# Kernel optimization log

Measured on AMD Instinct MI355X. Metric: run time of the kernel, lower is better.

The kernel has to match this reference:

```python
import jax, jax.numpy as jnp
import numpy as np

SEG_NUM = 100000
D_SEG = 128
D_S = 258       # 2*D_SEG + 2 (offset)
D_M7 = 512
D_M8 = 256
MASK = 64
T_SLOTS = 96
B = 4096
CAND_OUT = 4            # candidate_layer out_features
DW_COLS = D_M8 - CAND_OUT  # 252
BN_EPS = 1e-6
COS_EPS = 1e-8


def setup_inputs() -> dict:
    key = jax.random.key(0)
    ks = jax.random.split(key, 20)
    s = 0.02
    return {
        "src": jax.random.randint(ks[0], (B,), 0, SEG_NUM),
        "dest": jax.random.randint(ks[1], (B,), 0, SEG_NUM),
        "t": jax.random.randint(ks[2], (B,), 0, T_SLOTS),
        "candidates": jax.random.randint(ks[3], (B, MASK), 0, SEG_NUM),
        "offset": jax.random.normal(ks[4], (B, 4), jnp.float32),
        "emb_feat": jax.random.normal(ks[5], (SEG_NUM, D_SEG), jnp.float32) * s,
        "emb_dest": jax.random.normal(ks[6], (SEG_NUM, D_SEG), jnp.float32) * s,
        "w1": jax.random.normal(ks[7], (D_M7, D_S), jnp.float32) * s,
        "b1": jnp.zeros((D_M7,), jnp.float32),
        "bn_gamma": jnp.ones((D_M7,), jnp.float32),
        "bn_beta": jnp.zeros((D_M7,), jnp.float32),
        "bn_mean": jax.random.normal(ks[8], (D_M7,), jnp.float32) * s,
        "bn_var": jax.random.uniform(ks[9], (D_M7,), jnp.float32, 0.5, 1.5),
        "w2": jax.random.normal(ks[10], (D_M8, D_M7), jnp.float32) * s,
        "b2": jnp.zeros((D_M8,), jnp.float32),
        "dense_w": jax.random.normal(ks[11], (SEG_NUM, DW_COLS), jnp.float32) * s,
        "dense_b": jnp.zeros((SEG_NUM,), jnp.float32),
        "cand_w": jax.random.normal(ks[12], (CAND_OUT, 2), jnp.float32) * s,
        "cand_b": jnp.zeros((CAND_OUT,), jnp.float32),
        "segs_src": jax.random.normal(ks[13], (SEG_NUM, 2), jnp.float32),
        "segs_trg": jax.random.normal(ks[14], (SEG_NUM, 2), jnp.float32),
        "traffic_pop": jax.random.uniform(ks[15], (SEG_NUM, T_SLOTS), jnp.float32),
    }


def reference(src, dest, t, candidates, offset, emb_feat, emb_dest, w1, b1,
              bn_gamma, bn_beta, bn_mean, bn_var, w2, b2, dense_w, dense_b,
              cand_w, cand_b, segs_src, segs_trg, traffic_pop):
    # --- ODEncoder: embedding gathers + offset features ---
    code = jnp.concatenate([emb_feat[src], emb_dest[dest], offset[:, 1:3]], axis=1)  # [B, 258]
    # --- MLP: Linear -> BatchNorm1d (eval, running stats) -> ReLU -> Linear ---
    h = code @ w1.T + b1
    h = (h - bn_mean) * (bn_gamma / jnp.sqrt(bn_var + BN_EPS)) + bn_beta
    h = jax.nn.relu(h)
    out = h @ w2.T + b2  # [B, 256]
    # --- gather dense rows by candidate index ---
    sub_w = dense_w[candidates]   # [B, M, 252]
    sub_b = dense_b[candidates]   # [B, M]
    # --- traffic feature: traffic_pop[candidate, t] ---
    traffic_feat = traffic_pop[candidates, t[:, None]]  # [B, M]
    # --- cosine similarity between dest-direction and segment direction ---
    v1 = segs_src[dest][:, None, :] - segs_src[candidates]  # [B, M, 2]
    v2 = segs_trg[candidates] - segs_src[candidates]        # [B, M, 2]
    num = jnp.sum(v1 * v2, axis=-1)
    den = jnp.maximum(jnp.linalg.norm(v1, axis=-1) * jnp.linalg.norm(v2, axis=-1), COS_EPS)
    cos_feat = num / den  # [B, M]
    cand_feat = jnp.stack([cos_feat, traffic_feat], axis=-1)  # [B, M, 2]
    emb_cand = cand_feat @ cand_w.T + cand_b                  # [B, M, 4]
    W = jnp.concatenate([sub_w, emb_cand], axis=-1)           # [B, M, 256]
    # --- batched small matvec + bias ---
    logits = jnp.einsum('bmd,bd->bm', W, out) + sub_b         # [B, M]
    return logits
```

## Files before the change

### kernel.cpp

```cpp
#include <hip/hip_runtime.h>


#define BATCH 4096
#define DSEG 128
#define DS_ 258
#define DM7 512
#define DM8 256
#define NCAND 64
#define DWC 252
#define TSLOTS 96

typedef short bf16x8 __attribute__((ext_vector_type(8)));
typedef float f32x4 __attribute__((ext_vector_type(4)));

static __device__ __forceinline__ short f2bf(float f) {
    union { float f; unsigned u; } v; v.f = f;
    unsigned r = (v.u + 0x7FFFu + ((v.u >> 16) & 1u)) >> 16;
    return (short)r;
}

__global__ __launch_bounds__(512) void mlp_mfma_kernel(
    const int* __restrict__ src, const int* __restrict__ dest,
    const float* __restrict__ offset,
    const float* __restrict__ emb_feat, const float* __restrict__ emb_dest,
    const float* __restrict__ w1, const float* __restrict__ b1,
    const float* __restrict__ bn_gamma, const float* __restrict__ bn_beta,
    const float* __restrict__ bn_mean, const float* __restrict__ bn_var,
    const float* __restrict__ w2, const float* __restrict__ b2,
    float* __restrict__ out_ws)
{
    __shared__ __align__(16) short hlds[16][520];
    const int tid = threadIdx.x;
    const int w    = tid >> 6;
    const int lane = tid & 63;
    const int lg   = lane >> 4;
    const int lr   = lane & 15;
    const int b0   = blockIdx.x * 16;

    const int si = src[b0 + lr];
    const int di = dest[b0 + lr];
    const float* fb = emb_feat + (size_t)si * DSEG;
    const float* db = emb_dest + (size_t)di * DSEG;
    bf16x8 a1[8];
#pragma unroll
    for (int s = 0; s < 8; ++s) {
        const float* p = (s < 4) ? (fb + s * 32 + lg * 8)
                                 : (db + (s - 4) * 32 + lg * 8);
        const float4 x = *(const float4*)p;
        const float4 y = *(const float4*)(p + 4);
        bf16x8 t;
        t[0] = f2bf(x.x); t[1] = f2bf(x.y); t[2] = f2bf(x.z); t[3] = f2bf(x.w);
        t[4] = f2bf(y.x); t[5] = f2bf(y.y); t[6] = f2bf(y.z); t[7] = f2bf(y.w);
        a1[s] = t;
    }
    float off1[4], off2[4];
#pragma unroll
    for (int q = 0; q < 4; ++q) {
        const float4 o = *(const float4*)(offset + (size_t)(b0 + lg * 4 + q) * 4);
        off1[q] = o.y; off2[q] = o.z;
    }

#pragma unroll
    for (int nt = 0; nt < 4; ++nt) {
        const int n = (w * 4 + nt) * 16 + lr;
        const float* wrow = w1 + (size_t)n * DS_;
        f32x4 acc = {0.f, 0.f, 0.f, 0.f};
#pragma unroll
        for (int s = 0; s < 8; ++s) {
            const float* p = wrow + s * 32 + lg * 8;
            const float2 x0 = *(const float2*)(p);
            const float2 x1 = *(const float2*)(p + 2);
            const float2 x2 = *(const float2*)(p + 4);
            const float2 x3 = *(const float2*)(p + 6);
            bf16x8 bb;
            bb[0] = f2bf(x0.x); bb[1] = f2bf(x0.y); bb[2] = f2bf(x1.x); bb[3] = f2bf(x1.y);
            bb[4] = f2bf(x2.x); bb[5] = f2bf(x2.y); bb[6] = f2bf(x3.x); bb[7] = f2bf(x3.y);
            acc = __builtin_amdgcn_mfma_f32_16x16x32_bf16(a1[s], bb, acc, 0, 0, 0);
        }
        const float2 wtail = *(const float2*)(wrow + 256);
        const float scale = bn_gamma[n] / sqrtf(bn_var[n] + 1e-6f);
        const float shift = bn_beta[n] - bn_mean[n] * scale;
        const float bias  = b1[n];
#pragma unroll
        for (int q = 0; q < 4; ++q) {
            float v = acc[q] + bias + off1[q] * wtail.x + off2[q] * wtail.y;
            v = fmaf(v, scale, shift);
            v = fmaxf(v, 0.f);
            hlds[lg * 4 + q][n] = f2bf(v);
        }
    }
    __syncthreads();

    bf16x8 a2[16];
#pragma unroll
    for (int s = 0; s < 16; ++s) {
        a2[s] = *(const bf16x8*)&hlds[lr][s * 32 + lg * 8];
    }
#pragma unroll
    for (int nt = 0; nt < 2; ++nt) {
        const int n = (w * 2 + nt) * 16 + lr;
        const float* wrow = w2 + (size_t)n * DM7;
        f32x4 acc = {0.f, 0.f, 0.f, 0.f};
#pragma unroll
        for (int s = 0; s < 16; ++s) {
            const float4 x = *(const float4*)(wrow + s * 32 + lg * 8);
            const float4 y = *(const float4*)(wrow + s * 32 + lg * 8 + 4);
            bf16x8 bb;
            bb[0] = f2bf(x.x); bb[1] = f2bf(x.y); bb[2] = f2bf(x.z); bb[3] = f2bf(x.w);
            bb[4] = f2bf(y.x); bb[5] = f2bf(y.y); bb[6] = f2bf(y.z); bb[7] = f2bf(y.w);
            acc = __builtin_amdgcn_mfma_f32_16x16x32_bf16(a2[s], bb, acc, 0, 0, 0);
        }
        const float bias = b2[n];
#pragma unroll
        for (int q = 0; q < 4; ++q) {
            out_ws[(size_t)(b0 + lg * 4 + q) * DM8 + n] = acc[q] + bias;
        }
    }
}

__global__ __launch_bounds__(256) void logits_kernel(
    const int* __restrict__ dest, const int* __restrict__ tt,
    const int* __restrict__ candidates,
    const float* __restrict__ dense_w, const float* __restrict__ dense_b,
    const float* __restrict__ cand_w, const float* __restrict__ cand_b,
    const float* __restrict__ segs_src, const float* __restrict__ segs_trg,
    const float* __restrict__ traffic_pop,
    const float* __restrict__ out_ws,
    float* __restrict__ logits)
{
    __shared__ float plds[4][16][67];
    const int b = blockIdx.x;
    const int tid = threadIdx.x;
    const int wave = tid >> 6;
    const int lane = tid & 63;
    const int mbase = wave * 16;

    int candv = 0;
    if (lane < 16) candv = candidates[b * NCAND + mbase + lane];

    const int ll = (lane < 63) ? lane : 62;
    float4 dw[16];
#pragma unroll
    for (int i = 0; i < 16; ++i) {
        const int ci = __shfl(candv, i, 64);
        dw[i] = *(const float4*)(dense_w + (size_t)ci * DWC + ll * 4);
    }

    float4 o4 = *(const float4*)(out_ws + (size_t)b * DM8 + ll * 4);
    if (lane == 63) { o4.x = 0.f; o4.y = 0.f; o4.z = 0.f; o4.w = 0.f; }

    float tail = 0.f;
    if (lane < 16) {
        const float4 t4 = *(const float4*)(out_ws + (size_t)b * DM8 + DWC);
        const int db = dest[b];
        const float2 dsx = *(const float2*)(segs_src + 2 * (size_t)db);
        const float2 sx = *(const float2*)(segs_src + 2 * (size_t)candv);
        const float2 tx = *(const float2*)(segs_trg + 2 * (size_t)candv);
        const float v1x = dsx.x - sx.x, v1y = dsx.y - sx.y;
        const float v2x = tx.x - sx.x, v2y = tx.y - sx.y;
        const float num = v1x * v2x + v1y * v2y;
        const float den = fmaxf(sqrtf(v1x * v1x + v1y * v1y) *
                                sqrtf(v2x * v2x + v2y * v2y), 1e-8f);
        const float cosv = num / den;
        const float tf = traffic_pop[(size_t)candv * TSLOTS + tt[b]];
        const float e0 = fmaf(cosv, cand_w[0], fmaf(tf, cand_w[1], cand_b[0]));
        const float e1 = fmaf(cosv, cand_w[2], fmaf(tf, cand_w[3], cand_b[1]));
        const float e2 = fmaf(cosv, cand_w[4], fmaf(tf, cand_w[5], cand_b[2]));
        const float e3 = fmaf(cosv, cand_w[6], fmaf(tf, cand_w[7], cand_b[3]));
        tail = e0 * t4.x + e1 * t4.y + e2 * t4.z + e3 * t4.w + dense_b[candv];
    }

#pragma unroll
    for (int i = 0; i < 16; ++i) {
        const float p = dw[i].x * o4.x + dw[i].y * o4.y + dw[i].z * o4.z + dw[i].w * o4.w;
        plds[wave][i][lane] = p;
    }
    __syncthreads();

    const int cc = lane >> 2;
    const int qq = lane & 3;
    float s = 0.f;
#pragma unroll
    for (int j = 0; j < 16; ++j) s += plds[wave][cc][qq * 16 + j];
    s += __shfl_xor(s, 1, 64);
    s += __shfl_xor(s, 2, 64);
    const float tl = __shfl(tail, cc, 64);
    if (qq == 0) logits[(size_t)b * NCAND + mbase + cc] = s + tl;
}

extern "C" void kernel_launch(void* const* d_in, const int* in_sizes, int n_in,
                              void* d_out, int out_size, void* d_ws, size_t ws_size,
                              hipStream_t stream) {
    const int*   src         = (const int*)d_in[0];
    const int*   dest        = (const int*)d_in[1];
    const int*   tt          = (const int*)d_in[2];
    const int*   candidates  = (const int*)d_in[3];
    const float* offset      = (const float*)d_in[4];
    const float* emb_feat    = (const float*)d_in[5];
    const float* emb_dest    = (const float*)d_in[6];
    const float* w1          = (const float*)d_in[7];
    const float* b1          = (const float*)d_in[8];
    const float* bn_gamma    = (const float*)d_in[9];
    const float* bn_beta     = (const float*)d_in[10];
    const float* bn_mean     = (const float*)d_in[11];
    const float* bn_var      = (const float*)d_in[12];
    const float* w2          = (const float*)d_in[13];
    const float* b2          = (const float*)d_in[14];
    const float* dense_w     = (const float*)d_in[15];
    const float* dense_b     = (const float*)d_in[16];
    const float* cand_w      = (const float*)d_in[17];
    const float* cand_b      = (const float*)d_in[18];
    const float* segs_src    = (const float*)d_in[19];
    const float* segs_trg    = (const float*)d_in[20];
    const float* traffic_pop = (const float*)d_in[21];

    float* out_ws = (float*)d_ws;
    float* logits = (float*)d_out;

    mlp_mfma_kernel<<<BATCH / 16, 512, 0, stream>>>(
        src, dest, offset, emb_feat, emb_dest,
        w1, b1, bn_gamma, bn_beta, bn_mean, bn_var, w2, b2, out_ws);

    logits_kernel<<<BATCH, 256, 0, stream>>>(
        dest, tt, candidates, dense_w, dense_b, cand_w, cand_b,
        segs_src, segs_trg, traffic_pop, out_ws, logits);
}
```

Baseline: 89.28 us.

## Convert dense_w table to bf16 in extra MLP blocks and gather bf16 rows

Extra blocks appended to the MLP kernel convert the whole dense_w table from fp32 to bf16 into workspace on every call. The logits kernel then gathers 8-byte bf16 rows instead of 16-byte fp32 rows, halving gather traffic. The cost is a full-table read and a half-size write each call, plus bf16 rounding error in the logits. It only runs when the workspace is large enough for the table.

```diff
diff --git a/kernel.cpp b/kernel.cpp
--- a/kernel.cpp
+++ b/kernel.cpp
@@ -9,8 +9,10 @@
 #define NCAND 64
 #define DWC 252
 #define TSLOTS 96
+#define SEGN 100000
 
 typedef short bf16x8 __attribute__((ext_vector_type(8)));
+typedef short bf16x4 __attribute__((ext_vector_type(4)));
 typedef float f32x4 __attribute__((ext_vector_type(4)));
 
 static __device__ __forceinline__ short f2bf(float f) {
@@ -18,8 +20,11 @@
     unsigned r = (v.u + 0x7FFFu + ((v.u >> 16) & 1u)) >> 16;
     return (short)r;
 }
-
-__global__ __launch_bounds__(512) void mlp_mfma_kernel(
+static __device__ __forceinline__ float bfu2f(unsigned u16hi) {
+    union { unsigned u; float f; } v; v.u = u16hi << 16; return v.f;
+}
+
+__global__ __launch_bounds__(512) void mlp_conv_kernel(
     const int* __restrict__ src, const int* __restrict__ dest,
     const float* __restrict__ offset,
     const float* __restrict__ emb_feat, const float* __restrict__ emb_dest,
@@ -27,10 +32,27 @@
     const float* __restrict__ bn_gamma, const float* __restrict__ bn_beta,
     const float* __restrict__ bn_mean, const float* __restrict__ bn_var,
     const float* __restrict__ w2, const float* __restrict__ b2,
+    const float* __restrict__ dense_w, short* __restrict__ wtab,
     float* __restrict__ out_ws)
 {
+    const int tid = threadIdx.x;
+
+    if (blockIdx.x >= BATCH / 16) {
+        const size_t nthr = (size_t)(gridDim.x - BATCH / 16) * 512;
+        const size_t g0 = (size_t)(blockIdx.x - BATCH / 16) * 512 + tid;
+        const float4* __restrict__ src4 = (const float4*)dense_w;
+        bf16x4* __restrict__ dst4 = (bf16x4*)wtab;
+        const size_t n4 = (size_t)SEGN * DWC / 4;
+        for (size_t i = g0; i < n4; i += nthr) {
+            const float4 v = src4[i];
+            bf16x4 s;
+            s[0] = f2bf(v.x); s[1] = f2bf(v.y); s[2] = f2bf(v.z); s[3] = f2bf(v.w);
+            dst4[i] = s;
+        }
+        return;
+    }
+
     __shared__ __align__(16) short hlds[16][520];
-    const int tid = threadIdx.x;
     const int w    = tid >> 6;
     const int lane = tid & 63;
     const int lg   = lane >> 4;
@@ -118,10 +140,12 @@
     }
 }
 
-__global__ __launch_bounds__(256) void logits_kernel(
+template <bool BF16TAB>
+__global__ __launch_bounds__(256) void logits_kernel_t(
     const int* __restrict__ dest, const int* __restrict__ tt,
     const int* __restrict__ candidates,
-    const float* __restrict__ dense_w, const float* __restrict__ dense_b,
+    const float* __restrict__ dense_w, const unsigned short* __restrict__ wtab,
+    const float* __restrict__ dense_b,
     const float* __restrict__ cand_w, const float* __restrict__ cand_b,
     const float* __restrict__ segs_src, const float* __restrict__ segs_trg,
     const float* __restrict__ traffic_pop,
@@ -139,11 +163,20 @@
     if (lane < 16) candv = candidates[b * NCAND + mbase + lane];
 
     const int ll = (lane < 63) ? lane : 62;
-    float4 dw[16];
-#pragma unroll
-    for (int i = 0; i < 16; ++i) {
-        const int ci = __shfl(candv, i, 64);
-        dw[i] = *(const float4*)(dense_w + (size_t)ci * DWC + ll * 4);
+    float4 dwf[16];
+    uint2  dwb[16];
+    if (BF16TAB) {
+#pragma unroll
+        for (int i = 0; i < 16; ++i) {
+            const int ci = __shfl(candv, i, 64);
+            dwb[i] = *(const uint2*)(wtab + (size_t)ci * DWC + ll * 4);
+        }
+    } else {
+#pragma unroll
+        for (int i = 0; i < 16; ++i) {
+            const int ci = __shfl(candv, i, 64);
+            dwf[i] = *(const float4*)(dense_w + (size_t)ci * DWC + ll * 4);
+        }
     }
 
     float4 o4 = *(const float4*)(out_ws + (size_t)b * DM8 + ll * 4);
@@ -172,7 +205,15 @@
 
 #pragma unroll
     for (int i = 0; i < 16; ++i) {
-        const float p = dw[i].x * o4.x + dw[i].y * o4.y + dw[i].z * o4.z + dw[i].w * o4.w;
+        float p;
+        if (BF16TAB) {
+            p =        bfu2f(dwb[i].x & 0xFFFFu)  * o4.x;
+            p = fmaf(  bfu2f(dwb[i].x >> 16),       o4.y, p);
+            p = fmaf(  bfu2f(dwb[i].y & 0xFFFFu),   o4.z, p);
+            p = fmaf(  bfu2f(dwb[i].y >> 16),       o4.w, p);
+        } else {
+            p = dwf[i].x * o4.x + dwf[i].y * o4.y + dwf[i].z * o4.z + dwf[i].w * o4.w;
+        }
         plds[wave][i][lane] = p;
     }
     __syncthreads();
@@ -215,13 +256,25 @@
     const float* traffic_pop = (const float*)d_in[21];
 
     float* out_ws = (float*)d_ws;
+    const size_t OUT_WS_BYTES = (size_t)BATCH * DM8 * 4;
+    const size_t WTAB_BYTES = (size_t)SEGN * DWC * 2;
+    short* wtab = (short*)((char*)d_ws + OUT_WS_BYTES);
+    const bool use_bf16 = ws_size >= OUT_WS_BYTES + WTAB_BYTES;
     float* logits = (float*)d_out;
 
-    mlp_mfma_kernel<<<BATCH / 16, 512, 0, stream>>>(
+    const int nblk = use_bf16 ? (BATCH / 16) * 2 : (BATCH / 16);
+    mlp_conv_kernel<<<nblk, 512, 0, stream>>>(
         src, dest, offset, emb_feat, emb_dest,
-        w1, b1, bn_gamma, bn_beta, bn_mean, bn_var, w2, b2, out_ws);
-
-    logits_kernel<<<BATCH, 256, 0, stream>>>(
-        dest, tt, candidates, dense_w, dense_b, cand_w, cand_b,
-        segs_src, segs_trg, traffic_pop, out_ws, logits);
-}
+        w1, b1, bn_gamma, bn_beta, bn_mean, bn_var, w2, b2,
+        dense_w, wtab, out_ws);
+
+    if (use_bf16) {
+        logits_kernel_t<true><<<BATCH, 256, 0, stream>>>(
+            dest, tt, candidates, dense_w, (const unsigned short*)wtab, dense_b,
+            cand_w, cand_b, segs_src, segs_trg, traffic_pop, out_ws, logits);
+    } else {
+        logits_kernel_t<false><<<BATCH, 256, 0, stream>>>(
+            dest, tt, candidates, dense_w, (const unsigned short*)wtab, dense_b,
+            cand_w, cand_b, segs_src, segs_trg, traffic_pop, out_ws, logits);
+    }
+}
```

Result: faster. 86.39 us (-3.2%).

## Partition dense_w rows across blocks and bucket candidate hits to stream gathers

Applied to the files above, without the earlier changes.

Replaces the per-batch-row logits kernel with 256 blocks that each own a contiguous range of dense_w rows. Every block scans the whole candidates array, collects the hits that fall in its range into an LDS list, and computes logits with a wave-wide reduction per hit. The aim is better locality for the dense_w gathers, since each block touches only its own slice. In exchange every block rereads the full 1 MB candidates array, the LDS atomics serialize, and any hits beyond LISTCAP are silently dropped, so correctness depends on the input distribution.

```diff
diff --git a/kernel.cpp b/kernel.cpp
--- a/kernel.cpp
+++ b/kernel.cpp
@@ -9,6 +9,11 @@
 #define NCAND 64
 #define DWC 252
 #define TSLOTS 96
+#define SEGN 100000
+#define SBLK 256
+#define STHR 1024
+#define ROWS_PER_BLK 391
+#define LISTCAP 2560
 
 typedef short bf16x8 __attribute__((ext_vector_type(8)));
 typedef float f32x4 __attribute__((ext_vector_type(4)));
@@ -19,7 +24,7 @@
     return (short)r;
 }
 
-__global__ __launch_bounds__(512) void mlp_mfma_kernel(
+__global__ __launch_bounds__(512) void mlp_kernel(
     const int* __restrict__ src, const int* __restrict__ dest,
     const float* __restrict__ offset,
     const float* __restrict__ emb_feat, const float* __restrict__ emb_dest,
@@ -118,7 +123,7 @@
     }
 }
 
-__global__ __launch_bounds__(256) void logits_kernel(
+__global__ __launch_bounds__(1024) void logits_stream_kernel(
     const int* __restrict__ dest, const int* __restrict__ tt,
     const int* __restrict__ candidates,
     const float* __restrict__ dense_w, const float* __restrict__ dense_b,
@@ -128,64 +133,99 @@
     const float* __restrict__ out_ws,
     float* __restrict__ logits)
 {
-    __shared__ float plds[4][16][67];
-    const int b = blockIdx.x;
+    __shared__ int nhits;
+    __shared__ unsigned list_i[LISTCAP];
+    __shared__ int      list_s[LISTCAP];
+    __shared__ float    list_t[LISTCAP];
     const int tid = threadIdx.x;
-    const int wave = tid >> 6;
-    const int lane = tid & 63;
-    const int mbase = wave * 16;
-
-    int candv = 0;
-    if (lane < 16) candv = candidates[b * NCAND + mbase + lane];
-
-    const int ll = (lane < 63) ? lane : 62;
-    float4 dw[16];
-#pragma unroll
-    for (int i = 0; i < 16; ++i) {
-        const int ci = __shfl(candv, i, 64);
-        dw[i] = *(const float4*)(dense_w + (size_t)ci * DWC + ll * 4);
-    }
-
-    float4 o4 = *(const float4*)(out_ws + (size_t)b * DM8 + ll * 4);
-    if (lane == 63) { o4.x = 0.f; o4.y = 0.f; o4.z = 0.f; o4.w = 0.f; }
-
-    float tail = 0.f;
-    if (lane < 16) {
+    if (tid == 0) nhits = 0;
+    __syncthreads();
+
+    const int r0 = blockIdx.x * ROWS_PER_BLK;
+    const int r1 = r0 + ROWS_PER_BLK;
+
+    const int4* __restrict__ c4p = (const int4*)candidates;
+    for (int base = 0; base < (BATCH * NCAND) / 4; base += STHR) {
+        const int4 c = c4p[base + tid];
+        const unsigned i0 = (unsigned)(base + tid) * 4u;
+        if (c.x >= r0 && c.x < r1) {
+            const int p = atomicAdd(&nhits, 1);
+            if (p < LISTCAP) { list_i[p] = i0;     list_s[p] = c.x; }
+        }
+        if (c.y >= r0 && c.y < r1) {
+            const int p = atomicAdd(&nhits, 1);
+            if (p < LISTCAP) { list_i[p] = i0 + 1; list_s[p] = c.y; }
+        }
+        if (c.z >= r0 && c.z < r1) {
+            const int p = atomicAdd(&nhits, 1);
+            if (p < LISTCAP) { list_i[p] = i0 + 2; list_s[p] = c.z; }
+        }
+        if (c.w >= r0 && c.w < r1) {
+            const int p = atomicAdd(&nhits, 1);
+            if (p < LISTCAP) { list_i[p] = i0 + 3; list_s[p] = c.w; }
+        }
+    }
+    __syncthreads();
+    const int nh = (nhits < LISTCAP) ? nhits : LISTCAP;
+
+    for (int e = tid; e < nh; e += STHR) {
+        const unsigned i = list_i[e];
+        const int s = list_s[e];
+        const int b = (int)(i >> 6);
         const float4 t4 = *(const float4*)(out_ws + (size_t)b * DM8 + DWC);
         const int db = dest[b];
         const float2 dsx = *(const float2*)(segs_src + 2 * (size_t)db);
-        const float2 sx = *(const float2*)(segs_src + 2 * (size_t)candv);
-        const float2 tx = *(const float2*)(segs_trg + 2 * (size_t)candv);
+        const float2 sx = *(const float2*)(segs_src + 2 * (size_t)s);
+        const float2 tx = *(const float2*)(segs_trg + 2 * (size_t)s);
         const float v1x = dsx.x - sx.x, v1y = dsx.y - sx.y;
         const float v2x = tx.x - sx.x, v2y = tx.y - sx.y;
         const float num = v1x * v2x + v1y * v2y;
         const float den = fmaxf(sqrtf(v1x * v1x + v1y * v1y) *
                                 sqrtf(v2x * v2x + v2y * v2y), 1e-8f);
         const float cosv = num / den;
-        const float tf = traffic_pop[(size_t)candv * TSLOTS + tt[b]];
+        const float tf = traffic_pop[(size_t)s * TSLOTS + tt[b]];
         const float e0 = fmaf(cosv, cand_w[0], fmaf(tf, cand_w[1], cand_b[0]));
         const float e1 = fmaf(cosv, cand_w[2], fmaf(tf, cand_w[3], cand_b[1]));
         const float e2 = fmaf(cosv, cand_w[4], fmaf(tf, cand_w[5], cand_b[2]));
         const float e3 = fmaf(cosv, cand_w[6], fmaf(tf, cand_w[7], cand_b[3]));
-        tail = e0 * t4.x + e1 * t4.y + e2 * t4.z + e3 * t4.w + dense_b[candv];
-    }
-
-#pragma unroll
-    for (int i = 0; i < 16; ++i) {
-        const float p = dw[i].x * o4.x + dw[i].y * o4.y + dw[i].z * o4.z + dw[i].w * o4.w;
-        plds[wave][i][lane] = p;
-    }
-    __syncthreads();
-
-    const int cc = lane >> 2;
-    const int qq = lane & 3;
-    float s = 0.f;
-#pragma unroll
-    for (int j = 0; j < 16; ++j) s += plds[wave][cc][qq * 16 + j];
-    s += __shfl_xor(s, 1, 64);
-    s += __shfl_xor(s, 2, 64);
-    const float tl = __shfl(tail, cc, 64);
-    if (qq == 0) logits[(size_t)b * NCAND + mbase + cc] = s + tl;
+        list_t[e] = e0 * t4.x + e1 * t4.y + e2 * t4.z + e3 * t4.w + dense_b[s];
+    }
+    __syncthreads();
+
+    const int wave = tid >> 6;
+    const int lane = tid & 63;
+    const int ll = (lane < 63) ? lane : 62;
+    for (int e0 = wave; e0 < nh; e0 += 32) {
+        const int e1 = e0 + 16;
+        const unsigned i0 = list_i[e0];
+        const int s0 = list_s[e0];
+        const int b0 = (int)(i0 >> 6);
+        const float4 dw0 = *(const float4*)(dense_w + (size_t)s0 * DWC + ll * 4);
+        const float4 o0  = *(const float4*)(out_ws + (size_t)b0 * DM8 + ll * 4);
+        unsigned i1 = 0; int s1 = 0, b1v = 0;
+        float4 dw1 = {0.f,0.f,0.f,0.f}, o1 = {0.f,0.f,0.f,0.f};
+        const bool has1 = (e1 < nh);
+        if (has1) {
+            i1 = list_i[e1];
+            s1 = list_s[e1];
+            b1v = (int)(i1 >> 6);
+            dw1 = *(const float4*)(dense_w + (size_t)s1 * DWC + ll * 4);
+            o1  = *(const float4*)(out_ws + (size_t)b1v * DM8 + ll * 4);
+        }
+        float p0 = (lane == 63) ? list_t[e0]
+                 : dw0.x * o0.x + dw0.y * o0.y + dw0.z * o0.z + dw0.w * o0.w;
+        float p1 = (has1 && lane == 63) ? list_t[e1]
+                 : dw1.x * o1.x + dw1.y * o1.y + dw1.z * o1.z + dw1.w * o1.w;
+#pragma unroll
+        for (int sft = 1; sft < 64; sft <<= 1) {
+            p0 += __shfl_xor(p0, sft, 64);
+            p1 += __shfl_xor(p1, sft, 64);
+        }
+        if (lane == 0) {
+            logits[i0] = p0;
+            if (has1) logits[i1] = p1;
+        }
+    }
 }
 
 extern "C" void kernel_launch(void* const* d_in, const int* in_sizes, int n_in,
@@ -217,11 +257,11 @@
     float* out_ws = (float*)d_ws;
     float* logits = (float*)d_out;
 
-    mlp_mfma_kernel<<<BATCH / 16, 512, 0, stream>>>(
+    mlp_kernel<<<BATCH / 16, 512, 0, stream>>>(
         src, dest, offset, emb_feat, emb_dest,
         w1, b1, bn_gamma, bn_beta, bn_mean, bn_var, w2, b2, out_ws);
 
-    logits_kernel<<<BATCH, 256, 0, stream>>>(
+    logits_stream_kernel<<<SBLK, STHR, 0, stream>>>(
         dest, tt, candidates, dense_w, dense_b, cand_w, cand_b,
         segs_src, segs_trg, traffic_pop, out_ws, logits);
 }
```

After: 112.5 us. 1.26x slower.
